# Optimization experiments

Measured on AMD Instinct MI355X. Metric: run time of the kernel, lower is better.

Reference implementation:

```python
import jax, jax.numpy as jnp
import numpy as np

EMBED = 768
HEADS = 12
HDIM = EMBED // HEADS
FF = EMBED * 2
B, LQ, LK = 4, 2048, 2048


def _linear(x, W, b):
    # W: [in, out]
    return x @ W + b


def _layernorm(x, g, b, eps=1e-5):
    mu = jnp.mean(x, axis=-1, keepdims=True)
    var = jnp.mean(jnp.square(x - mu), axis=-1, keepdims=True)
    return (x - mu) * jax.lax.rsqrt(var + eps) * g + b


def _l2norm(x, eps=1e-12):
    # matches F.normalize: x / max(||x||_2, eps)
    n = jnp.sqrt(jnp.sum(jnp.square(x), axis=-1, keepdims=True))
    return x / jnp.maximum(n, eps)


def _heads(x):
    b, l, _ = x.shape
    return x.reshape(b, l, HEADS, HDIM).transpose(0, 2, 1, 3)  # [B,H,L,hd]


def setup_inputs() -> dict:
    key = jax.random.key(0)
    ks = jax.random.split(key, 20)
    s = 0.02
    d = {
        'image_tokens': jax.random.normal(ks[0], (B, LQ, EMBED), jnp.float32),
        'point_tokens': jax.random.normal(ks[1], (B, LK, EMBED), jnp.float32),
        'image_pos': jax.random.normal(ks[2], (B, LQ, EMBED), jnp.float32),
        'point_pos': jax.random.normal(ks[3], (B, LK, EMBED), jnp.float32),
        'Wip': jax.random.normal(ks[4], (EMBED, EMBED), jnp.float32) * s,
        'bip': jnp.zeros((EMBED,), jnp.float32),
        'Wpp': jax.random.normal(ks[5], (EMBED, EMBED), jnp.float32) * s,
        'bpp': jnp.zeros((EMBED,), jnp.float32),
        'Wq': jax.random.normal(ks[6], (EMBED, EMBED), jnp.float32) * s,
        'bq': jnp.zeros((EMBED,), jnp.float32),
        'Wk': jax.random.normal(ks[7], (EMBED, EMBED), jnp.float32) * s,
        'bk': jnp.zeros((EMBED,), jnp.float32),
        'Wv': jax.random.normal(ks[8], (EMBED, EMBED), jnp.float32) * s,
        'bv': jnp.zeros((EMBED,), jnp.float32),
        'Wo': jax.random.normal(ks[9], (EMBED, EMBED), jnp.float32) * s,
        'bo': jnp.zeros((EMBED,), jnp.float32),
        'g1': jnp.ones((EMBED,), jnp.float32),
        'b1': jnp.zeros((EMBED,), jnp.float32),
        'g2': jnp.ones((EMBED,), jnp.float32),
        'b2': jnp.zeros((EMBED,), jnp.float32),
        'Wf1': jax.random.normal(ks[10], (EMBED, FF), jnp.float32) * s,
        'bf1': jnp.zeros((FF,), jnp.float32),
        'Wf2': jax.random.normal(ks[11], (FF, EMBED), jnp.float32) * s,
        'bf2': jnp.zeros((EMBED,), jnp.float32),
    }
    return d


def reference(image_tokens, point_tokens, image_pos, point_pos,
              Wip, bip, Wpp, bpp, Wq, bq, Wk, bk, Wv, bv, Wo, bo,
              g1, b1, g2, b2, Wf1, bf1, Wf2, bf2):
    q = _linear(image_tokens + _linear(image_pos, Wip, bip), Wq, bq)
    k = _linear(point_tokens + _linear(point_pos, Wpp, bpp), Wk, bk)
    v = _linear(point_tokens, Wv, bv)

    q = _l2norm(_heads(q))  # [B,H,Lq,hd]
    k = _l2norm(_heads(k))  # [B,H,Lk,hd]
    v = _heads(v)           # [B,H,Lk,hd]

    scores = jnp.einsum('bhqd,bhkd->bhqk', q, k)
    attn = jax.nn.softmax(scores, axis=-1)
    fused = jnp.einsum('bhqk,bhkd->bhqd', attn, v)
    fused = fused.transpose(0, 2, 1, 3).reshape(image_tokens.shape[0], image_tokens.shape[1], EMBED)

    fused = _layernorm(image_tokens + _linear(fused, Wo, bo), g1, b1)
    h = _linear(fused, Wf1, bf1)
    h = 0.5 * h * (1.0 + jax.lax.erf(h / jnp.sqrt(jnp.float32(2.0))))  # exact GELU
    ff = _linear(h, Wf2, bf2)
    return _layernorm(fused + ff, g2, b2)
```

## Files before the change

kernel.cpp:

```cpp
#include <hip/hip_runtime.h>

#define EMBED 768
#define FFDIM 1536
#define BATCH 4
#define SEQ   2048
#define HEADS 12
#define MROWS (BATCH*SEQ)

typedef __attribute__((ext_vector_type(4))) float  f32x4;
typedef __attribute__((ext_vector_type(8))) __bf16 bf16x8;
typedef __attribute__((ext_vector_type(4))) short  s16x4;

__device__ __forceinline__ short f2bf(float f) {
    union { float f; unsigned u; } x; x.f = f;
    unsigned r = x.u + 0x7fffu + ((x.u >> 16) & 1u);
    return (short)(r >> 16);
}

__device__ __forceinline__ void gll16(const void* g, void* l) {
    __builtin_amdgcn_global_load_lds(
        (const __attribute__((address_space(1))) void*)g,
        (__attribute__((address_space(3))) void*)l, 16, 0, 0);
}

__device__ __forceinline__ bf16x8 ldsw(const short* base, int row, int chunk) {
    return *(const bf16x8*)((const char*)base + row * 128 + (((chunk ^ (row & 7))) << 4));
}

__global__ __launch_bounds__(256) void cvt4_kernel(
    const float* __restrict__ s0, const float* __restrict__ s1,
    const float* __restrict__ s2, const float* __restrict__ s3,
    short* __restrict__ o0, short* __restrict__ o1,
    short* __restrict__ o2, short* __restrict__ o3)
{
    const float* s; short* o;
    switch (blockIdx.y) {
        case 0:  s = s0; o = o0; break;
        case 1:  s = s1; o = o1; break;
        case 2:  s = s2; o = o2; break;
        default: s = s3; o = o3; break;
    }
    size_t i = ((size_t)blockIdx.x * 256 + threadIdx.x) * 4;
    float4 v = *(const float4*)(s + i);
    s16x4 r;
    r[0] = f2bf(v.x); r[1] = f2bf(v.y); r[2] = f2bf(v.z); r[3] = f2bf(v.w);
    *(s16x4*)(o + i) = r;
}

__global__ __launch_bounds__(256) void transpose_w(
    const float* __restrict__ W, short* __restrict__ Wt, int K, int N)
{
    __shared__ float tile[32][33];
    const int k0 = blockIdx.y * 32, n0 = blockIdx.x * 32;
    const int tx = threadIdx.x & 31, ty = threadIdx.x >> 5;
    #pragma unroll
    for (int i = 0; i < 32; i += 8)
        tile[ty + i][tx] = W[(size_t)(k0 + ty + i) * N + n0 + tx];
    __syncthreads();
    #pragma unroll
    for (int i = 0; i < 32; i += 8)
        Wt[(size_t)(n0 + ty + i) * K + k0 + tx] = f2bf(tile[tx][ty + i]);
}

__global__ __launch_bounds__(256) void transpose_v(
    const short* __restrict__ v, short* __restrict__ vt)
{
    __shared__ short tile[64][65];
    const int bh = blockIdx.y;
    const int b = bh / HEADS, h = bh % HEADS;
    const int k0 = blockIdx.x * 64;
    const int tx = threadIdx.x & 63, ty = threadIdx.x >> 6;
    #pragma unroll
    for (int i = 0; i < 64; i += 4)
        tile[ty + i][tx] = v[(size_t)(b * SEQ + k0 + ty + i) * EMBED + h * 64 + tx];
    __syncthreads();
    #pragma unroll
    for (int i = 0; i < 64; i += 4)
        vt[(size_t)(bh * 64 + ty + i) * SEQ + k0 + tx] = tile[tx][ty + i];
}

template<int L2N, int GELU_, int RES, int SBF, int SF32>
__global__ __launch_bounds__(256) void gemm_bt(
    const short* __restrict__ A, const short* __restrict__ Wt,
    const float* __restrict__ bias, const float* __restrict__ resid,
    short* __restrict__ outb, float* __restrict__ outf,
    int M, int N, int K)
{
    __shared__ short As[2][128][32];
    __shared__ short Bs[2][128][32];
    const int tid = threadIdx.x;
    const int mbase = blockIdx.y * 128, nbase = blockIdx.x * 128;
    const int wid = tid >> 6, lane = tid & 63;
    const int wm = wid >> 1, wn = wid & 1;
    const int l15 = lane & 15, lhi = lane >> 4;
    const int sr = tid >> 2;
    const int sc = (tid & 3) * 8;

    f32x4 acc[4][4] = {};

    const short* Ab = A  + (size_t)mbase * K;
    const short* Bb = Wt + (size_t)nbase * K;

#define GSTAGE(buf, kk)                                                         \
    gll16(Ab + (size_t)sr * K        + (kk) + sc, &As[buf][sr][sc]);            \
    gll16(Ab + (size_t)(64 + sr) * K + (kk) + sc, &As[buf][64 + sr][sc]);       \
    gll16(Bb + (size_t)sr * K        + (kk) + sc, &Bs[buf][sr][sc]);            \
    gll16(Bb + (size_t)(64 + sr) * K + (kk) + sc, &Bs[buf][64 + sr][sc]);

    GSTAGE(0, 0);
    __syncthreads();

    const int nk = K >> 5;
    for (int t = 0; t < nk; ++t) {
        const int cur = t & 1;
        if (t + 1 < nk) { GSTAGE(cur ^ 1, (t + 1) << 5); }
        bf16x8 av[4], bv[4];
        #pragma unroll
        for (int tt = 0; tt < 4; ++tt) {
            av[tt] = *(const bf16x8*)(&As[cur][wm * 64 + tt * 16 + l15][lhi * 8]);
            bv[tt] = *(const bf16x8*)(&Bs[cur][wn * 64 + tt * 16 + l15][lhi * 8]);
        }
        #pragma unroll
        for (int mt = 0; mt < 4; ++mt)
            #pragma unroll
            for (int nt = 0; nt < 4; ++nt)
                acc[mt][nt] = __builtin_amdgcn_mfma_f32_16x16x32_bf16(
                    av[mt], bv[nt], acc[mt][nt], 0, 0, 0);
        __syncthreads();
    }
#undef GSTAGE

    #pragma unroll
    for (int mt = 0; mt < 4; ++mt) {
        float vals[4][4];
        #pragma unroll
        for (int nt = 0; nt < 4; ++nt) {
            const int col = nbase + wn * 64 + nt * 16 + l15;
            const float bc = bias[col];
            #pragma unroll
            for (int j = 0; j < 4; ++j) vals[nt][j] = acc[mt][nt][j] + bc;
        }
        if (RES) {
            #pragma unroll
            for (int nt = 0; nt < 4; ++nt) {
                const int col = nbase + wn * 64 + nt * 16 + l15;
                #pragma unroll
                for (int j = 0; j < 4; ++j) {
                    const int row = mbase + wm * 64 + mt * 16 + lhi * 4 + j;
                    vals[nt][j] += resid[(size_t)row * N + col];
                }
            }
        }
        if (L2N) {
            #pragma unroll
            for (int j = 0; j < 4; ++j) {
                float s = 0.f;
                #pragma unroll
                for (int nt = 0; nt < 4; ++nt) s += vals[nt][j] * vals[nt][j];
                s += __shfl_xor(s, 1); s += __shfl_xor(s, 2);
                s += __shfl_xor(s, 4); s += __shfl_xor(s, 8);
                const float inv = 1.0f / fmaxf(sqrtf(s), 1e-12f);
                #pragma unroll
                for (int nt = 0; nt < 4; ++nt) vals[nt][j] *= inv;
            }
        }
        if (GELU_) {
            #pragma unroll
            for (int nt = 0; nt < 4; ++nt)
                #pragma unroll
                for (int j = 0; j < 4; ++j) {
                    const float v = vals[nt][j];
                    vals[nt][j] = 0.5f * v * (1.0f + erff(v * 0.70710678118654752f));
                }
        }
        #pragma unroll
        for (int nt = 0; nt < 4; ++nt) {
            const int col = nbase + wn * 64 + nt * 16 + l15;
            #pragma unroll
            for (int j = 0; j < 4; ++j) {
                const int row = mbase + wm * 64 + mt * 16 + lhi * 4 + j;
                if (SBF)  outb[(size_t)row * N + col] = f2bf(vals[nt][j]);
                if (SF32) outf[(size_t)row * N + col] = vals[nt][j];
            }
        }
    }
}

__global__ __launch_bounds__(512) void attn_kernel(
    const short* __restrict__ qn, const short* __restrict__ kn,
    const short* __restrict__ vt, short* __restrict__ outp)
{
    __shared__ short Qs[128][64];
    __shared__ short Ks[2][64][64];
    __shared__ short Vs[2][64][64];
    __shared__ short Ps[128][64];

    const int bh = blockIdx.y;
    const int b = bh / HEADS, h = bh % HEADS;
    const int q0 = blockIdx.x * 128;
    const int tid = threadIdx.x, wid = tid >> 6, lane = tid & 63;
    const int l15 = lane & 15, lhi = lane >> 4;
    const int srow = tid >> 3;
    const int schk = tid & 7;

    #pragma unroll
    for (int p = 0; p < 2; ++p) {
        const int cid = p * 512 + tid;
        const int r = cid >> 3, c = cid & 7;
        gll16(qn + (size_t)(b * SEQ + q0 + r) * EMBED + h * 64 + ((c ^ (r & 7)) * 8),
              &Qs[r][c * 8]);
    }
    gll16(kn + (size_t)(b * SEQ + srow) * EMBED + h * 64 + ((schk ^ (srow & 7)) * 8),
          &Ks[0][srow][schk * 8]);
    gll16(vt + (size_t)(bh * 64 + srow) * SEQ + ((schk ^ (srow & 7)) * 8),
          &Vs[0][srow][schk * 8]);
    __syncthreads();

    const bf16x8 aq0 = ldsw(&Qs[0][0], wid * 16 + l15, lhi);
    const bf16x8 aq1 = ldsw(&Qs[0][0], wid * 16 + l15, 4 + lhi);

    f32x4 acc_o[4] = {};
    float rowsum[4] = {0.f, 0.f, 0.f, 0.f};
    char* const ps_base = (char*)&Ps[0][0];

    for (int kt = 0; kt < SEQ / 64; ++kt) {
        const int cur = kt & 1;
        if (kt + 1 < SEQ / 64) {
            const int k0n = (kt + 1) * 64;
            gll16(kn + (size_t)(b * SEQ + k0n + srow) * EMBED + h * 64 + ((schk ^ (srow & 7)) * 8),
                  &Ks[cur ^ 1][srow][schk * 8]);
            gll16(vt + (size_t)(bh * 64 + srow) * SEQ + k0n + ((schk ^ (srow & 7)) * 8),
                  &Vs[cur ^ 1][srow][schk * 8]);
        }

        #pragma unroll
        for (int nt = 0; nt < 4; ++nt) {
            bf16x8 bk0 = ldsw(&Ks[cur][0][0], nt * 16 + l15, lhi);
            bf16x8 bk1 = ldsw(&Ks[cur][0][0], nt * 16 + l15, 4 + lhi);
            f32x4 s = {0.f, 0.f, 0.f, 0.f};
            s = __builtin_amdgcn_mfma_f32_16x16x32_bf16(aq0, bk0, s, 0, 0, 0);
            s = __builtin_amdgcn_mfma_f32_16x16x32_bf16(aq1, bk1, s, 0, 0, 0);
            #pragma unroll
            for (int j = 0; j < 4; ++j) {
                const float e = __expf(s[j]);
                rowsum[j] += e;
                const int q = wid * 16 + lhi * 4 + j;
                const int k = nt * 16 + l15;
                const int chunk = k >> 3;
                *(short*)(ps_base + q * 128 + ((chunk ^ (q & 7)) << 4) + (k & 7) * 2) = f2bf(e);
            }
        }

        #pragma unroll
        for (int ks = 0; ks < 2; ++ks) {
            bf16x8 ap = ldsw(&Ps[0][0], wid * 16 + l15, ks * 4 + lhi);
            #pragma unroll
            for (int dt = 0; dt < 4; ++dt) {
                bf16x8 bvv = ldsw(&Vs[cur][0][0], dt * 16 + l15, ks * 4 + lhi);
                acc_o[dt] = __builtin_amdgcn_mfma_f32_16x16x32_bf16(ap, bvv, acc_o[dt], 0, 0, 0);
            }
        }
        __syncthreads();
    }

    #pragma unroll
    for (int j = 0; j < 4; ++j) {
        float s = rowsum[j];
        s += __shfl_xor(s, 1); s += __shfl_xor(s, 2);
        s += __shfl_xor(s, 4); s += __shfl_xor(s, 8);
        rowsum[j] = s;
    }

    #pragma unroll
    for (int dt = 0; dt < 4; ++dt)
        #pragma unroll
        for (int j = 0; j < 4; ++j) {
            const int row = q0 + wid * 16 + lhi * 4 + j;
            const int col = h * 64 + dt * 16 + l15;
            outp[(size_t)(b * SEQ + row) * EMBED + col] = f2bf(acc_o[dt][j] / rowsum[j]);
        }
}

template<int SBF>
__global__ __launch_bounds__(256) void layernorm_768(
    const float* __restrict__ x, const float* __restrict__ g, const float* __restrict__ bb,
    float* __restrict__ outf, short* __restrict__ outb)
{
    const int row = blockIdx.x;
    const float* xr = x + (size_t)row * EMBED;
    const int t = threadIdx.x;
    const float v0 = xr[t], v1 = xr[t + 256], v2 = xr[t + 512];
    float s = v0 + v1 + v2;
    #pragma unroll
    for (int m = 1; m < 64; m <<= 1) s += __shfl_xor(s, m);
    __shared__ float red[4];
    __shared__ float red2[4];
    const int wid = t >> 6, lane = t & 63;
    if (lane == 0) red[wid] = s;
    __syncthreads();
    const float mu = (red[0] + red[1] + red[2] + red[3]) * (1.0f / 768.0f);
    const float d0 = v0 - mu, d1 = v1 - mu, d2 = v2 - mu;
    float ss = d0 * d0 + d1 * d1 + d2 * d2;
    #pragma unroll
    for (int m = 1; m < 64; m <<= 1) ss += __shfl_xor(ss, m);
    if (lane == 0) red2[wid] = ss;
    __syncthreads();
    const float var = (red2[0] + red2[1] + red2[2] + red2[3]) * (1.0f / 768.0f);
    const float inv = rsqrtf(var + 1e-5f);
    const float y0 = d0 * inv * g[t] + bb[t];
    const float y1 = d1 * inv * g[t + 256] + bb[t + 256];
    const float y2 = d2 * inv * g[t + 512] + bb[t + 512];
    float* of = outf + (size_t)row * EMBED;
    of[t] = y0; of[t + 256] = y1; of[t + 512] = y2;
    if (SBF) {
        short* ob = outb + (size_t)row * EMBED;
        ob[t] = f2bf(y0); ob[t + 256] = f2bf(y1); ob[t + 512] = f2bf(y2);
    }
}

extern "C" void kernel_launch(void* const* d_in, const int* in_sizes, int n_in,
                              void* d_out, int out_size, void* d_ws, size_t ws_size,
                              hipStream_t stream)
{
    (void)in_sizes; (void)n_in; (void)out_size; (void)ws_size;
    const float* itok = (const float*)d_in[0];
    const float* ptok = (const float*)d_in[1];
    const float* ipos = (const float*)d_in[2];
    const float* ppos = (const float*)d_in[3];
    const float* Wip = (const float*)d_in[4];  const float* bip = (const float*)d_in[5];
    const float* Wpp = (const float*)d_in[6];  const float* bpp = (const float*)d_in[7];
    const float* Wq  = (const float*)d_in[8];  const float* bq  = (const float*)d_in[9];
    const float* Wk  = (const float*)d_in[10]; const float* bk  = (const float*)d_in[11];
    const float* Wv  = (const float*)d_in[12]; const float* bv  = (const float*)d_in[13];
    const float* Wo  = (const float*)d_in[14]; const float* bo  = (const float*)d_in[15];
    const float* g1  = (const float*)d_in[16]; const float* b1  = (const float*)d_in[17];
    const float* g2  = (const float*)d_in[18]; const float* b2  = (const float*)d_in[19];
    const float* Wf1 = (const float*)d_in[20]; const float* bf1 = (const float*)d_in[21];
    const float* Wf2 = (const float*)d_in[22]; const float* bf2 = (const float*)d_in[23];
    float* out = (float*)d_out;

    char* ws = (char*)d_ws;
    constexpr size_t SZ_BF  = (size_t)MROWS * EMBED * 2;
    constexpr size_t SZ_F32 = (size_t)MROWS * EMBED * 4;
    constexpr size_t W768B  = (size_t)EMBED * EMBED * 2;
    constexpr size_t W1536B = (size_t)EMBED * FFDIM * 2;

    size_t o = 0;
    short* it_bf    = (short*)(ws + o); o += SZ_BF;
    short* pt_bf    = (short*)(ws + o); o += SZ_BF;
    short* ip_bf    = (short*)(ws + o); o += SZ_BF;
    short* pp_bf    = (short*)(ws + o); o += SZ_BF;
    short* qin_bf   = (short*)(ws + o); o += SZ_BF;
    short* kin_bf   = (short*)(ws + o); o += SZ_BF;
    short* qn_bf    = (short*)(ws + o); o += SZ_BF;
    short* kn_bf    = (short*)(ws + o); o += SZ_BF;
    short* attn_bf  = (short*)(ws + o); o += SZ_BF;
    float* x_f32    = (float*)(ws + o); o += SZ_F32;
    short* fused_bf = (short*)(ws + o); o += SZ_BF;
    float* fused_f32= (float*)(ws + o); o += SZ_F32;
    short* wip_t = (short*)(ws + o); o += W768B;
    short* wpp_t = (short*)(ws + o); o += W768B;
    short* wq_t  = (short*)(ws + o); o += W768B;
    short* wk_t  = (short*)(ws + o); o += W768B;
    short* wv_t  = (short*)(ws + o); o += W768B;
    short* wo_t  = (short*)(ws + o); o += W768B;
    short* wf1_t = (short*)(ws + o); o += W1536B;
    short* wf2_t = (short*)(ws + o); o += W1536B;
    short* v_bf  = ip_bf;
    short* vt_bf = pp_bf;
    short* h_bf  = qin_bf;

    const dim3 blk(256);

    cvt4_kernel<<<dim3(MROWS * EMBED / 1024, 4), blk, 0, stream>>>(
        itok, ptok, ipos, ppos, it_bf, pt_bf, ip_bf, pp_bf);

    transpose_w<<<dim3(EMBED / 32, EMBED / 32), blk, 0, stream>>>(Wip, wip_t, EMBED, EMBED);
    transpose_w<<<dim3(EMBED / 32, EMBED / 32), blk, 0, stream>>>(Wpp, wpp_t, EMBED, EMBED);
    transpose_w<<<dim3(EMBED / 32, EMBED / 32), blk, 0, stream>>>(Wq,  wq_t,  EMBED, EMBED);
    transpose_w<<<dim3(EMBED / 32, EMBED / 32), blk, 0, stream>>>(Wk,  wk_t,  EMBED, EMBED);
    transpose_w<<<dim3(EMBED / 32, EMBED / 32), blk, 0, stream>>>(Wv,  wv_t,  EMBED, EMBED);
    transpose_w<<<dim3(EMBED / 32, EMBED / 32), blk, 0, stream>>>(Wo,  wo_t,  EMBED, EMBED);
    transpose_w<<<dim3(FFDIM / 32, EMBED / 32), blk, 0, stream>>>(Wf1, wf1_t, EMBED, FFDIM);
    transpose_w<<<dim3(EMBED / 32, FFDIM / 32), blk, 0, stream>>>(Wf2, wf2_t, FFDIM, EMBED);

    const dim3 g768(EMBED / 128, MROWS / 128);
    const dim3 g1536(FFDIM / 128, MROWS / 128);

    gemm_bt<0,0,1,1,0><<<g768, blk, 0, stream>>>(ip_bf, wip_t, bip, itok, qin_bf, nullptr, MROWS, EMBED, EMBED);
    gemm_bt<0,0,1,1,0><<<g768, blk, 0, stream>>>(pp_bf, wpp_t, bpp, ptok, kin_bf, nullptr, MROWS, EMBED, EMBED);
    gemm_bt<1,0,0,1,0><<<g768, blk, 0, stream>>>(qin_bf, wq_t, bq, nullptr, qn_bf, nullptr, MROWS, EMBED, EMBED);
    gemm_bt<1,0,0,1,0><<<g768, blk, 0, stream>>>(kin_bf, wk_t, bk, nullptr, kn_bf, nullptr, MROWS, EMBED, EMBED);
    gemm_bt<0,0,0,1,0><<<g768, blk, 0, stream>>>(pt_bf, wv_t, bv, nullptr, v_bf, nullptr, MROWS, EMBED, EMBED);

    transpose_v<<<dim3(SEQ / 64, BATCH * HEADS), blk, 0, stream>>>(v_bf, vt_bf);
    attn_kernel<<<dim3(SEQ / 128, BATCH * HEADS), dim3(512), 0, stream>>>(qn_bf, kn_bf, vt_bf, attn_bf);

    gemm_bt<0,0,1,0,1><<<g768, blk, 0, stream>>>(attn_bf, wo_t, bo, itok, nullptr, x_f32, MROWS, EMBED, EMBED);
    layernorm_768<1><<<dim3(MROWS), blk, 0, stream>>>(x_f32, g1, b1, fused_f32, fused_bf);
    gemm_bt<0,1,0,1,0><<<g1536, blk, 0, stream>>>(fused_bf, wf1_t, bf1, nullptr, h_bf, nullptr, MROWS, FFDIM, EMBED);
    gemm_bt<0,0,1,0,1><<<g768, blk, 0, stream>>>(h_bf, wf2_t, bf2, fused_f32, nullptr, x_f32, MROWS, EMBED, FFDIM);
    layernorm_768<0><<<dim3(MROWS), blk, 0, stream>>>(x_f32, g2, b2, out, nullptr);
}
```

Baseline: 561.3 us.

## Rewrite attention with 32x32 MFMA and register-resident P; batch projection GEMMs

The attention kernel moves from 16x16x32 to 32x32x16 MFMA tiles with 256 threads. Each wave keeps Q fragments in registers and computes S transposed (K as the A operand), so the exp'd probabilities can be packed to bf16 with v_cvt_pk and swapped across half-waves instead of going through a shared-memory P buffer. Output is staged through LDS for coalesced 16-byte stores. Separately, the five projection GEMMs are merged into two launches (3-way and 2-way via blockIdx.z), and the unused image_tokens bf16 conversion is dropped. The risks are the cross-lane shuffle cost and higher register pressure from two 16-float accumulators plus exp temporaries.

```diff
diff --git a/kernel.cpp b/kernel.cpp
--- a/kernel.cpp
+++ b/kernel.cpp
@@ -7,9 +7,10 @@
 #define HEADS 12
 #define MROWS (BATCH*SEQ)
 
-typedef __attribute__((ext_vector_type(4))) float  f32x4;
-typedef __attribute__((ext_vector_type(8))) __bf16 bf16x8;
-typedef __attribute__((ext_vector_type(4))) short  s16x4;
+typedef __attribute__((ext_vector_type(4)))  float  f32x4;
+typedef __attribute__((ext_vector_type(16))) float  f32x16;
+typedef __attribute__((ext_vector_type(8)))  __bf16 bf16x8;
+typedef __attribute__((ext_vector_type(4)))  short  s16x4;
 
 __device__ __forceinline__ short f2bf(float f) {
     union { float f; unsigned u; } x; x.f = f;
@@ -17,6 +18,12 @@
     return (short)(r >> 16);
 }
 
+__device__ __forceinline__ unsigned cvtpk(float lo, float hi) {
+    unsigned r;
+    asm("v_cvt_pk_bf16_f32 %0, %1, %2" : "=v"(r) : "v"(lo), "v"(hi));
+    return r;
+}
+
 __device__ __forceinline__ void gll16(const void* g, void* l) {
     __builtin_amdgcn_global_load_lds(
         (const __attribute__((address_space(1))) void*)g,
@@ -27,18 +34,16 @@
     return *(const bf16x8*)((const char*)base + row * 128 + (((chunk ^ (row & 7))) << 4));
 }
 
-__global__ __launch_bounds__(256) void cvt4_kernel(
+__global__ __launch_bounds__(256) void cvt3_kernel(
     const float* __restrict__ s0, const float* __restrict__ s1,
-    const float* __restrict__ s2, const float* __restrict__ s3,
-    short* __restrict__ o0, short* __restrict__ o1,
-    short* __restrict__ o2, short* __restrict__ o3)
+    const float* __restrict__ s2,
+    short* __restrict__ o0, short* __restrict__ o1, short* __restrict__ o2)
 {
     const float* s; short* o;
     switch (blockIdx.y) {
         case 0:  s = s0; o = o0; break;
         case 1:  s = s1; o = o1; break;
-        case 2:  s = s2; o = o2; break;
-        default: s = s3; o = o3; break;
+        default: s = s2; o = o2; break;
     }
     size_t i = ((size_t)blockIdx.x * 256 + threadIdx.x) * 4;
     float4 v = *(const float4*)(s + i);
@@ -79,12 +84,11 @@
         vt[(size_t)(bh * 64 + ty + i) * SEQ + k0 + tx] = tile[tx][ty + i];
 }
 
-template<int L2N, int GELU_, int RES, int SBF, int SF32>
-__global__ __launch_bounds__(256) void gemm_bt(
+template<int L2N, int GELU_, int SBF, int SF32>
+__device__ __forceinline__ void gemm_core(
     const short* __restrict__ A, const short* __restrict__ Wt,
     const float* __restrict__ bias, const float* __restrict__ resid,
-    short* __restrict__ outb, float* __restrict__ outf,
-    int M, int N, int K)
+    short* __restrict__ outb, float* __restrict__ outf, int N, int K)
 {
     __shared__ short As[2][128][32];
     __shared__ short Bs[2][128][32];
@@ -140,7 +144,7 @@
             #pragma unroll
             for (int j = 0; j < 4; ++j) vals[nt][j] = acc[mt][nt][j] + bc;
         }
-        if (RES) {
+        if (resid != nullptr) {
             #pragma unroll
             for (int nt = 0; nt < 4; ++nt) {
                 const int col = nbase + wn * 64 + nt * 16 + l15;
@@ -186,99 +190,158 @@
     }
 }
 
-__global__ __launch_bounds__(512) void attn_kernel(
+template<int L2N, int GELU_, int SBF, int SF32>
+__global__ __launch_bounds__(256) void gemm_bt(
+    const short* __restrict__ A, const short* __restrict__ Wt,
+    const float* __restrict__ bias, const float* __restrict__ resid,
+    short* __restrict__ outb, float* __restrict__ outf, int N, int K)
+{
+    gemm_core<L2N, GELU_, SBF, SF32>(A, Wt, bias, resid, outb, outf, N, K);
+}
+
+__global__ __launch_bounds__(256) void gemm3_kernel(
+    const short* A0, const short* W0, const float* b0, const float* r0, short* o0,
+    const short* A1, const short* W1, const float* b1, const float* r1, short* o1,
+    const short* A2, const short* W2, const float* b2, const float* r2, short* o2)
+{
+    const short *A, *W; const float *bi, *re; short* ob;
+    if (blockIdx.z == 0)      { A = A0; W = W0; bi = b0; re = r0; ob = o0; }
+    else if (blockIdx.z == 1) { A = A1; W = W1; bi = b1; re = r1; ob = o1; }
+    else                      { A = A2; W = W2; bi = b2; re = r2; ob = o2; }
+    gemm_core<0, 0, 1, 0>(A, W, bi, re, ob, nullptr, EMBED, EMBED);
+}
+
+__global__ __launch_bounds__(256) void gemm2_kernel(
+    const short* A0, const short* W0, const float* b0, short* o0,
+    const short* A1, const short* W1, const float* b1, short* o1)
+{
+    const short *A, *W; const float *bi; short* ob;
+    if (blockIdx.z == 0) { A = A0; W = W0; bi = b0; ob = o0; }
+    else                 { A = A1; W = W1; bi = b1; ob = o1; }
+    gemm_core<1, 0, 1, 0>(A, W, bi, nullptr, ob, nullptr, EMBED, EMBED);
+}
+
+__global__ __launch_bounds__(256) void attn_kernel(
     const short* __restrict__ qn, const short* __restrict__ kn,
     const short* __restrict__ vt, short* __restrict__ outp)
 {
-    __shared__ short Qs[128][64];
     __shared__ short Ks[2][64][64];
     __shared__ short Vs[2][64][64];
-    __shared__ short Ps[128][64];
 
     const int bh = blockIdx.y;
     const int b = bh / HEADS, h = bh % HEADS;
     const int q0 = blockIdx.x * 128;
-    const int tid = threadIdx.x, wid = tid >> 6, lane = tid & 63;
-    const int l15 = lane & 15, lhi = lane >> 4;
+    const int tid = threadIdx.x, wq = tid >> 6, lane = tid & 63;
+    const int l31 = lane & 31, hi = lane >> 5;
     const int srow = tid >> 3;
     const int schk = tid & 7;
 
+    const size_t qrow = (size_t)(b * SEQ + q0 + wq * 32 + l31) * EMBED + h * 64;
+    bf16x8 qf[4];
+    #pragma unroll
+    for (int t = 0; t < 4; ++t)
+        qf[t] = *(const bf16x8*)(qn + qrow + t * 16 + hi * 8);
+
+    const short* kbase = kn + (size_t)b * SEQ * EMBED + h * 64;
+    const short* vbase = vt + (size_t)bh * 64 * SEQ;
+
+#define ASTAGE(buf, k0x) do {                                                            \
+    _Pragma("unroll")                                                                    \
+    for (int rr = 0; rr < 2; ++rr) {                                                     \
+        const int row = rr * 32 + srow;                                                  \
+        gll16(kbase + (size_t)((k0x) + row) * EMBED + ((schk ^ (row & 7)) * 8),          \
+              &Ks[buf][row][schk * 8]);                                                  \
+        gll16(vbase + (size_t)row * SEQ + (k0x) + ((schk ^ (row & 7)) * 8),              \
+              &Vs[buf][row][schk * 8]);                                                  \
+    }                                                                                    \
+} while (0)
+
+    ASTAGE(0, 0);
+    __syncthreads();
+
+    f32x16 acc_o[2] = {};
+    float rsum = 0.f;
+    const int NT = SEQ / 64;
+
+    for (int kt = 0; kt < NT; ++kt) {
+        const int cur = kt & 1;
+        if (kt + 1 < NT) { ASTAGE(cur ^ 1, (kt + 1) * 64); }
+
+        f32x16 s0 = {}, s1 = {};
+        #pragma unroll
+        for (int t = 0; t < 4; ++t) {
+            bf16x8 kf0 = ldsw(&Ks[cur][0][0], l31,      t * 2 + hi);
+            bf16x8 kf1 = ldsw(&Ks[cur][0][0], 32 + l31, t * 2 + hi);
+            s0 = __builtin_amdgcn_mfma_f32_32x32x16_bf16(kf0, qf[t], s0, 0, 0, 0);
+            s1 = __builtin_amdgcn_mfma_f32_32x32x16_bf16(kf1, qf[t], s1, 0, 0, 0);
+        }
+
+        float e0[16], e1[16];
+        #pragma unroll
+        for (int i = 0; i < 16; ++i) { const float e = __expf(s0[i]); rsum += e; e0[i] = e; }
+        #pragma unroll
+        for (int i = 0; i < 16; ++i) { const float e = __expf(s1[i]); rsum += e; e1[i] = e; }
+
+        unsigned w[2][8], sw[2][8];
+        #pragma unroll
+        for (int a = 0; a < 4; ++a) {
+            w[0][2*a]   = cvtpk(e0[4*a],   e0[4*a+1]);
+            w[0][2*a+1] = cvtpk(e0[4*a+2], e0[4*a+3]);
+            w[1][2*a]   = cvtpk(e1[4*a],   e1[4*a+1]);
+            w[1][2*a+1] = cvtpk(e1[4*a+2], e1[4*a+3]);
+        }
+        #pragma unroll
+        for (int kb = 0; kb < 2; ++kb)
+            #pragma unroll
+            for (int i = 0; i < 8; ++i)
+                sw[kb][i] = (unsigned)__shfl_xor((int)w[kb][i], 32);
+
+        #pragma unroll
+        for (int kb = 0; kb < 2; ++kb) {
+            #pragma unroll
+            for (int ks = 0; ks < 2; ++ks) {
+                union { unsigned u[4]; bf16x8 v; } pf;
+                pf.u[0] = hi ? sw[kb][4*ks+2] : w[kb][4*ks];
+                pf.u[1] = hi ? sw[kb][4*ks+3] : w[kb][4*ks+1];
+                pf.u[2] = hi ? w[kb][4*ks+2]  : sw[kb][4*ks];
+                pf.u[3] = hi ? w[kb][4*ks+3]  : sw[kb][4*ks+1];
+                #pragma unroll
+                for (int db = 0; db < 2; ++db) {
+                    bf16x8 vf = ldsw(&Vs[cur][0][0], db * 32 + l31, kb * 4 + ks * 2 + hi);
+                    acc_o[db] = __builtin_amdgcn_mfma_f32_32x32x16_bf16(vf, pf.v, acc_o[db], 0, 0, 0);
+                }
+            }
+        }
+        __syncthreads();
+    }
+#undef ASTAGE
+
+    const float rtot = rsum + __shfl_xor(rsum, 32);
+    const float rinv = 1.0f / rtot;
+
+    short* Osb = &Ks[0][0][0];
+    const int ql = wq * 32 + l31;
+    #pragma unroll
+    for (int db = 0; db < 2; ++db)
+        #pragma unroll
+        for (int a = 0; a < 4; ++a) {
+            const float v0 = acc_o[db][4*a]   * rinv, v1 = acc_o[db][4*a+1] * rinv;
+            const float v2 = acc_o[db][4*a+2] * rinv, v3 = acc_o[db][4*a+3] * rinv;
+            uint2 pw; pw.x = cvtpk(v0, v1); pw.y = cvtpk(v2, v3);
+            const int byteoff = ql * 128 + (((db * 4 + a) ^ (ql & 7)) << 4) + hi * 8;
+            *(uint2*)((char*)Osb + byteoff) = pw;
+        }
+    __syncthreads();
     #pragma unroll
     for (int p = 0; p < 2; ++p) {
-        const int cid = p * 512 + tid;
-        const int r = cid >> 3, c = cid & 7;
-        gll16(qn + (size_t)(b * SEQ + q0 + r) * EMBED + h * 64 + ((c ^ (r & 7)) * 8),
-              &Qs[r][c * 8]);
-    }
-    gll16(kn + (size_t)(b * SEQ + srow) * EMBED + h * 64 + ((schk ^ (srow & 7)) * 8),
-          &Ks[0][srow][schk * 8]);
-    gll16(vt + (size_t)(bh * 64 + srow) * SEQ + ((schk ^ (srow & 7)) * 8),
-          &Vs[0][srow][schk * 8]);
-    __syncthreads();
-
-    const bf16x8 aq0 = ldsw(&Qs[0][0], wid * 16 + l15, lhi);
-    const bf16x8 aq1 = ldsw(&Qs[0][0], wid * 16 + l15, 4 + lhi);
-
-    f32x4 acc_o[4] = {};
-    float rowsum[4] = {0.f, 0.f, 0.f, 0.f};
-    char* const ps_base = (char*)&Ps[0][0];
-
-    for (int kt = 0; kt < SEQ / 64; ++kt) {
-        const int cur = kt & 1;
-        if (kt + 1 < SEQ / 64) {
-            const int k0n = (kt + 1) * 64;
-            gll16(kn + (size_t)(b * SEQ + k0n + srow) * EMBED + h * 64 + ((schk ^ (srow & 7)) * 8),
-                  &Ks[cur ^ 1][srow][schk * 8]);
-            gll16(vt + (size_t)(bh * 64 + srow) * SEQ + k0n + ((schk ^ (srow & 7)) * 8),
-                  &Vs[cur ^ 1][srow][schk * 8]);
-        }
-
-        #pragma unroll
-        for (int nt = 0; nt < 4; ++nt) {
-            bf16x8 bk0 = ldsw(&Ks[cur][0][0], nt * 16 + l15, lhi);
-            bf16x8 bk1 = ldsw(&Ks[cur][0][0], nt * 16 + l15, 4 + lhi);
-            f32x4 s = {0.f, 0.f, 0.f, 0.f};
-            s = __builtin_amdgcn_mfma_f32_16x16x32_bf16(aq0, bk0, s, 0, 0, 0);
-            s = __builtin_amdgcn_mfma_f32_16x16x32_bf16(aq1, bk1, s, 0, 0, 0);
-            #pragma unroll
-            for (int j = 0; j < 4; ++j) {
-                const float e = __expf(s[j]);
-                rowsum[j] += e;
-                const int q = wid * 16 + lhi * 4 + j;
-                const int k = nt * 16 + l15;
-                const int chunk = k >> 3;
-                *(short*)(ps_base + q * 128 + ((chunk ^ (q & 7)) << 4) + (k & 7) * 2) = f2bf(e);
-            }
-        }
-
-        #pragma unroll
-        for (int ks = 0; ks < 2; ++ks) {
-            bf16x8 ap = ldsw(&Ps[0][0], wid * 16 + l15, ks * 4 + lhi);
-            #pragma unroll
-            for (int dt = 0; dt < 4; ++dt) {
-                bf16x8 bvv = ldsw(&Vs[cur][0][0], dt * 16 + l15, ks * 4 + lhi);
-                acc_o[dt] = __builtin_amdgcn_mfma_f32_16x16x32_bf16(ap, bvv, acc_o[dt], 0, 0, 0);
-            }
-        }
-        __syncthreads();
-    }
-
-    #pragma unroll
-    for (int j = 0; j < 4; ++j) {
-        float s = rowsum[j];
-        s += __shfl_xor(s, 1); s += __shfl_xor(s, 2);
-        s += __shfl_xor(s, 4); s += __shfl_xor(s, 8);
-        rowsum[j] = s;
-    }
-
-    #pragma unroll
-    for (int dt = 0; dt < 4; ++dt)
-        #pragma unroll
-        for (int j = 0; j < 4; ++j) {
-            const int row = q0 + wid * 16 + lhi * 4 + j;
-            const int col = h * 64 + dt * 16 + l15;
-            outp[(size_t)(b * SEQ + row) * EMBED + col] = f2bf(acc_o[dt][j] / rowsum[j]);
-        }
+        const int r = p * 64 + (tid >> 2);
+        #pragma unroll
+        for (int i = 0; i < 2; ++i) {
+            const int c = (tid & 3) * 2 + i;
+            bf16x8 v = ldsw(Osb, r, c);
+            *(bf16x8*)(outp + (size_t)(b * SEQ + q0 + r) * EMBED + h * 64 + c * 8) = v;
+        }
+    }
 }
 
 template<int SBF>
@@ -346,7 +409,7 @@
     constexpr size_t W1536B = (size_t)EMBED * FFDIM * 2;
 
     size_t o = 0;
-    short* it_bf    = (short*)(ws + o); o += SZ_BF;
+    short* v_bf     = (short*)(ws + o); o += SZ_BF;
     short* pt_bf    = (short*)(ws + o); o += SZ_BF;
     short* ip_bf    = (short*)(ws + o); o += SZ_BF;
     short* pp_bf    = (short*)(ws + o); o += SZ_BF;
@@ -366,14 +429,13 @@
     short* wo_t  = (short*)(ws + o); o += W768B;
     short* wf1_t = (short*)(ws + o); o += W1536B;
     short* wf2_t = (short*)(ws + o); o += W1536B;
-    short* v_bf  = ip_bf;
     short* vt_bf = pp_bf;
     short* h_bf  = qin_bf;
 
     const dim3 blk(256);
 
-    cvt4_kernel<<<dim3(MROWS * EMBED / 1024, 4), blk, 0, stream>>>(
-        itok, ptok, ipos, ppos, it_bf, pt_bf, ip_bf, pp_bf);
+    cvt3_kernel<<<dim3(MROWS * EMBED / 1024, 3), blk, 0, stream>>>(
+        ptok, ipos, ppos, pt_bf, ip_bf, pp_bf);
 
     transpose_w<<<dim3(EMBED / 32, EMBED / 32), blk, 0, stream>>>(Wip, wip_t, EMBED, EMBED);
     transpose_w<<<dim3(EMBED / 32, EMBED / 32), blk, 0, stream>>>(Wpp, wpp_t, EMBED, EMBED);
@@ -384,21 +446,21 @@
     transpose_w<<<dim3(FFDIM / 32, EMBED / 32), blk, 0, stream>>>(Wf1, wf1_t, EMBED, FFDIM);
     transpose_w<<<dim3(EMBED / 32, FFDIM / 32), blk, 0, stream>>>(Wf2, wf2_t, FFDIM, EMBED);
 
-    const dim3 g768(EMBED / 128, MROWS / 128);
-    const dim3 g1536(FFDIM / 128, MROWS / 128);
-
-    gemm_bt<0,0,1,1,0><<<g768, blk, 0, stream>>>(ip_bf, wip_t, bip, itok, qin_bf, nullptr, MROWS, EMBED, EMBED);
-    gemm_bt<0,0,1,1,0><<<g768, blk, 0, stream>>>(pp_bf, wpp_t, bpp, ptok, kin_bf, nullptr, MROWS, EMBED, EMBED);
-    gemm_bt<1,0,0,1,0><<<g768, blk, 0, stream>>>(qin_bf, wq_t, bq, nullptr, qn_bf, nullptr, MROWS, EMBED, EMBED);
-    gemm_bt<1,0,0,1,0><<<g768, blk, 0, stream>>>(kin_bf, wk_t, bk, nullptr, kn_bf, nullptr, MROWS, EMBED, EMBED);
-    gemm_bt<0,0,0,1,0><<<g768, blk, 0, stream>>>(pt_bf, wv_t, bv, nullptr, v_bf, nullptr, MROWS, EMBED, EMBED);
+    gemm3_kernel<<<dim3(6, 64, 3), blk, 0, stream>>>(
+        ip_bf, wip_t, bip, itok, qin_bf,
+        pp_bf, wpp_t, bpp, ptok, kin_bf,
+        pt_bf, wv_t,  bv,  nullptr, v_bf);
+
+    gemm2_kernel<<<dim3(6, 64, 2), blk, 0, stream>>>(
+        qin_bf, wq_t, bq, qn_bf,
+        kin_bf, wk_t, bk, kn_bf);
 
     transpose_v<<<dim3(SEQ / 64, BATCH * HEADS), blk, 0, stream>>>(v_bf, vt_bf);
-    attn_kernel<<<dim3(SEQ / 128, BATCH * HEADS), dim3(512), 0, stream>>>(qn_bf, kn_bf, vt_bf, attn_bf);
-
-    gemm_bt<0,0,1,0,1><<<g768, blk, 0, stream>>>(attn_bf, wo_t, bo, itok, nullptr, x_f32, MROWS, EMBED, EMBED);
+    attn_kernel<<<dim3(SEQ / 128, BATCH * HEADS), blk, 0, stream>>>(qn_bf, kn_bf, vt_bf, attn_bf);
+
+    gemm_bt<0,0,0,1><<<dim3(6, 64), blk, 0, stream>>>(attn_bf, wo_t, bo, itok, nullptr, x_f32, EMBED, EMBED);
     layernorm_768<1><<<dim3(MROWS), blk, 0, stream>>>(x_f32, g1, b1, fused_f32, fused_bf);
-    gemm_bt<0,1,0,1,0><<<g1536, blk, 0, stream>>>(fused_bf, wf1_t, bf1, nullptr, h_bf, nullptr, MROWS, FFDIM, EMBED);
-    gemm_bt<0,0,1,0,1><<<g768, blk, 0, stream>>>(h_bf, wf2_t, bf2, fused_f32, nullptr, x_f32, MROWS, EMBED, FFDIM);
+    gemm_bt<0,1,1,0><<<dim3(12, 64), blk, 0, stream>>>(fused_bf, wf1_t, bf1, nullptr, h_bf, nullptr, FFDIM, EMBED);
+    gemm_bt<0,0,0,1><<<dim3(6, 64), blk, 0, stream>>>(h_bf, wf2_t, bf2, fused_f32, nullptr, x_f32, EMBED, FFDIM);
     layernorm_768<0><<<dim3(MROWS), blk, 0, stream>>>(x_f32, g2, b2, out, nullptr);
 }
```

Measured after the change: 519.4 us. 7.5% less time.
